# Performance work log

Hardware: AMD Instinct MI355X
Metric: run time of the kernel (lower is better)

## Reference

```python
import jax, jax.numpy as jnp
import numpy as np

B, S, D, H = 2, 2048, 1024, 16
HD = D // H  # head size = 64

def setup_inputs() -> dict:
    key = jax.random.key(0)
    ks = jax.random.split(key, 12)
    sc = 0.02
    return {
        "hidden_states": jax.random.normal(ks[0], (B, S, D), jnp.float32),
        "attention_mask": jnp.zeros((B, S), jnp.float32),  # additive mask (0 = attend)
        "position_bias": jax.random.normal(ks[1], (H, S, S), jnp.float32) * sc,
        "Wq": jax.random.normal(ks[2], (D, D), jnp.float32) * sc,
        "bq": jnp.zeros((D,), jnp.float32),
        "Wk": jax.random.normal(ks[3], (D, D), jnp.float32) * sc,
        "bk": jnp.zeros((D,), jnp.float32),
        "Wv": jax.random.normal(ks[4], (D, D), jnp.float32) * sc,
        "bv": jnp.zeros((D,), jnp.float32),
        "Wo": jax.random.normal(ks[5], (D, D), jnp.float32) * sc,
        "bo": jnp.zeros((D,), jnp.float32),
    }

def reference(hidden_states, attention_mask, position_bias, Wq, bq, Wk, bk, Wv, bv, Wo, bo):
    b, s, _ = hidden_states.shape
    def heads(x):
        # [B,S,D] -> [B,H,S,HD]
        return x.reshape(b, s, H, HD).transpose(0, 2, 1, 3)
    q = heads(hidden_states @ Wq + bq)
    k = heads(hidden_states @ Wk + bk)
    v = heads(hidden_states @ Wv + bv)
    scores = jnp.einsum("bhqd,bhkd->bhqk", q, k) / jnp.sqrt(jnp.float32(HD))
    scores = scores + position_bias[None]                 # [1,H,S,S]
    scores = scores + attention_mask[:, None, None, :]    # [B,1,1,S]
    probs = jax.nn.softmax(scores, axis=-1)
    # dropout is identity in eval mode
    ctx = jnp.einsum("bhqk,bhkd->bhqd", probs, v)
    ctx = ctx.transpose(0, 2, 1, 3).reshape(b, s, D)
    return ctx @ Wo + bo
```

## Files before the change

### kernel.cpp

```cpp
#include <hip/hip_runtime.h>
#include <hip/hip_bf16.h>

#define B_  2
#define S_  2048
#define D_  1024
#define H_  16
#define HD_ 64
#define M_  (B_ * S_)

typedef unsigned short u16;
typedef __attribute__((ext_vector_type(8))) short short8;
typedef __attribute__((ext_vector_type(4))) float f32x4;

#define MFMA16(a, b, c) __builtin_amdgcn_mfma_f32_16x16x32_bf16(a, b, c, 0, 0, 0)

__device__ __forceinline__ u16 f2bf(float f) {
    union { float f; unsigned u; } v; v.f = f;
    unsigned r = v.u + 0x7FFFu + ((v.u >> 16) & 1u);
    return (u16)(r >> 16);
}

__device__ __forceinline__ void gl_lds16(const void* g, void* lds) {
    __builtin_amdgcn_global_load_lds(
        (const __attribute__((address_space(1))) unsigned int*)g,
        (__attribute__((address_space(3))) unsigned int*)lds, 16, 0, 0);
}

__global__ __launch_bounds__(256) void cvt_bf16(const float* __restrict__ x,
                                                u16* __restrict__ y) {
    const int i = (blockIdx.x * 256 + threadIdx.x) * 4;
    const float4 v = *(const float4*)(x + i);
    ushort4 o;
    o.x = f2bf(v.x); o.y = f2bf(v.y); o.z = f2bf(v.z); o.w = f2bf(v.w);
    *(ushort4*)(y + i) = o;
}

__global__ __launch_bounds__(256) void wt_trans(
    const float* __restrict__ w0, const float* __restrict__ w1,
    const float* __restrict__ w2, const float* __restrict__ w3,
    u16* __restrict__ t0, u16* __restrict__ t1,
    u16* __restrict__ t2, u16* __restrict__ t3) {
    const float* W; u16* T;
    switch (blockIdx.z) {
        case 0: W = w0; T = t0; break;
        case 1: W = w1; T = t1; break;
        case 2: W = w2; T = t2; break;
        default: W = w3; T = t3; break;
    }
    __shared__ float t[32][33];
    const int tid = threadIdx.x;
    const int kt = blockIdx.x, nt = blockIdx.y;
    const int r = tid >> 3, c4 = (tid & 7) * 4;
    const float4 v = *(const float4*)&W[(size_t)(kt * 32 + r) * D_ + nt * 32 + c4];
    t[c4 + 0][r] = v.x; t[c4 + 1][r] = v.y; t[c4 + 2][r] = v.z; t[c4 + 3][r] = v.w;
    __syncthreads();
    ushort4 o;
    o.x = f2bf(t[r][c4 + 0]); o.y = f2bf(t[r][c4 + 1]);
    o.z = f2bf(t[r][c4 + 2]); o.w = f2bf(t[r][c4 + 3]);
    *(ushort4*)&T[(size_t)(nt * 32 + r) * D_ + kt * 32 + c4] = o;
}

__global__ __launch_bounds__(256) void v_trans(const u16* __restrict__ V,
                                               u16* __restrict__ VT) {
    __shared__ u16 t[64][72];
    const int bh = blockIdx.x, s0 = blockIdx.y * 64;
    const int tid = threadIdx.x;
    const int ss = tid >> 2, cq = tid & 3;
    const u16* src = V + ((size_t)bh * S_ + s0 + ss) * HD_ + cq * 16;
    u16 buf[16];
    *(uint4*)&buf[0] = *(const uint4*)&src[0];
    *(uint4*)&buf[8] = *(const uint4*)&src[8];
#pragma unroll
    for (int j = 0; j < 16; ++j) t[cq * 16 + j][ss] = buf[j];
    __syncthreads();
    const int dd = tid >> 2;
    u16 ob[16];
#pragma unroll
    for (int j = 0; j < 16; ++j) ob[j] = t[dd][cq * 16 + j];
    u16* dst = VT + ((size_t)bh * HD_ + dd) * S_ + s0 + cq * 16;
    *(uint4*)&dst[0] = *(uint4*)&ob[0];
    *(uint4*)&dst[8] = *(uint4*)&ob[8];
}

__global__ __launch_bounds__(256, 3) void gemm_bt_bf16(
    const u16* __restrict__ A, const u16* __restrict__ Bt,
    const float* __restrict__ bi0, const float* __restrict__ bi1, const float* __restrict__ bi2,
    void* __restrict__ o0, void* __restrict__ o1, void* __restrict__ o2,
    int mode) {
    __shared__ __align__(16) char smem[32768];

    const int tid = threadIdx.x;
    const int wave = tid >> 6, lane = tid & 63;
    const int quad = lane >> 4, l15 = lane & 15;
    const int wm = wave >> 1, wn = wave & 1;
    const int bm = blockIdx.x * 128, bn = blockIdx.y * 128;

    const int sel = bn >> 10;
    const float* bias = (sel == 0) ? bi0 : (sel == 1) ? bi1 : bi2;
    void* outp = (sel == 0) ? o0 : (sel == 1) ? o1 : o2;

    f32x4 acc[4][4];
#pragma unroll
    for (int i = 0; i < 4; ++i)
#pragma unroll
        for (int j = 0; j < 4; ++j) acc[i][j] = (f32x4)0.f;

    const int c0 = wave * 128 + lane;
#pragma unroll
    for (int i = 0; i < 2; ++i) {
        const int c = c0 + i * 64;
        const int row = c >> 2, e = c & 3;
        gl_lds16(A  + (size_t)(bm + row) * D_ + e * 8,
                 smem + (wave * 2 + i) * 1024);
        gl_lds16(Bt + (size_t)(bn + row) * D_ + e * 8,
                 smem + 16384 + (wave * 2 + i) * 1024);
    }
    __syncthreads();

    for (int it = 0; it < 32; ++it) {
        const int cur = it & 1;
        if (it < 31) {
            const int k0n = (it + 1) * 32;
            const int nb = cur ^ 1;
#pragma unroll
            for (int i = 0; i < 2; ++i) {
                const int c = c0 + i * 64;
                const int row = c >> 2, e = c & 3;
                gl_lds16(A  + (size_t)(bm + row) * D_ + k0n + e * 8,
                         smem + nb * 8192 + (wave * 2 + i) * 1024);
                gl_lds16(Bt + (size_t)(bn + row) * D_ + k0n + e * 8,
                         smem + 16384 + nb * 8192 + (wave * 2 + i) * 1024);
            }
        }

        short8 aF[4], bF[4];
#pragma unroll
        for (int mt = 0; mt < 4; ++mt)
            aF[mt] = *(const short8*)(smem + cur * 8192 +
                     ((wm * 64 + mt * 16 + l15) * 32 + quad * 8) * 2);
#pragma unroll
        for (int nt = 0; nt < 4; ++nt)
            bF[nt] = *(const short8*)(smem + 16384 + cur * 8192 +
                     ((wn * 64 + nt * 16 + l15) * 32 + quad * 8) * 2);
#pragma unroll
        for (int mt = 0; mt < 4; ++mt)
#pragma unroll
            for (int nt = 0; nt < 4; ++nt)
                acc[mt][nt] = MFMA16(aF[mt], bF[nt], acc[mt][nt]);

        __syncthreads();
    }

    float bv[4];
#pragma unroll
    for (int nt = 0; nt < 4; ++nt)
        bv[nt] = bias[(bn & 1023) + wn * 64 + nt * 16 + l15];

    if (mode == 1) {
        u16* ob = (u16*)outp;
#pragma unroll
        for (int mt = 0; mt < 4; ++mt)
#pragma unroll
            for (int nt = 0; nt < 4; ++nt)
#pragma unroll
                for (int r = 0; r < 4; ++r) {
                    const int m = bm + wm * 64 + mt * 16 + quad * 4 + r;
                    const int n = (bn & 1023) + wn * 64 + nt * 16 + l15;
                    const int bb = m >> 11, ss = m & (S_ - 1);
                    const int hh = n >> 6,  dd = n & (HD_ - 1);
                    ob[(((size_t)bb * H_ + hh) * S_ + ss) * HD_ + dd] =
                        f2bf(acc[mt][nt][r] + bv[nt]);
                }
    } else {
        float* of = (float*)outp;
#pragma unroll
        for (int mt = 0; mt < 4; ++mt)
#pragma unroll
            for (int nt = 0; nt < 4; ++nt)
#pragma unroll
                for (int r = 0; r < 4; ++r) {
                    const int m = bm + wm * 64 + mt * 16 + quad * 4 + r;
                    const int n = bn + wn * 64 + nt * 16 + l15;
                    of[(size_t)m * D_ + n] = acc[mt][nt][r] + bv[nt];
                }
    }
}

#define AQP_OFF 0
#define AK_OFF  8192
#define AV_OFF  24576

__global__ __launch_bounds__(256, 4) void attn_mfma(
    const u16* __restrict__ Qg, const u16* __restrict__ Kg, const u16* __restrict__ VTg,
    const float* __restrict__ pb, const float* __restrict__ mask,
    u16* __restrict__ Cb) {
    __shared__ __align__(16) char smem[40960];
    u16* PsU = (u16*)(smem + AQP_OFF);

    const int tid = threadIdx.x;
    const int wave = tid >> 6, lane = tid & 63;
    const int quad = lane >> 4, l15 = lane & 15;

    const int b = blockIdx.x & 1, qblk = blockIdx.x >> 1;
    const int h = blockIdx.y;
    const int q0 = qblk * 64;

    const size_t bh = (size_t)b * H_ + h;
    const u16* Qb  = Qg  + bh * (S_ * HD_);
    const u16* Kb  = Kg  + bh * (S_ * HD_);
    const u16* VTb = VTg + bh * (HD_ * S_);

#pragma unroll
    for (int i = 0; i < 2; ++i) {
        const int c = (wave * 2 + i) * 64 + lane;
        const int row = c >> 3, e = c & 7, dc = e ^ (row & 7);
        gl_lds16(Qb + (size_t)(q0 + row) * HD_ + dc * 8,
                 smem + AQP_OFF + (wave * 2 + i) * 1024);
        gl_lds16(Kb + (size_t)row * HD_ + dc * 8,
                 smem + AK_OFF + (wave * 2 + i) * 1024);
        gl_lds16(VTb + (size_t)row * S_ + dc * 8,
                 smem + AV_OFF + (wave * 2 + i) * 1024);
    }
    __syncthreads();

    short8 aQ[2];
#pragma unroll
    for (int kc = 0; kc < 2; ++kc) {
        const int q = wave * 16 + l15;
        const int dc = kc * 4 + quad;
        aQ[kc] = *(const short8*)(smem + AQP_OFF + (q * 8 + (dc ^ (q & 7))) * 16);
    }

    u16* Pw = PsU + (l15 >> 3) * 512 + (wave * 16 + quad * 4) * 8 + (l15 & 7);

    f32x4 O[4];
    float lst[4];
#pragma unroll
    for (int nt = 0; nt < 4; ++nt) O[nt] = (f32x4)0.f;
#pragma unroll
    for (int r = 0; r < 4; ++r) lst[r] = 0.f;

    for (int kt = 0; kt < S_ / 64; ++kt) {
        const int k0 = kt * 64;
        const int cur = kt & 1;

        if (kt < S_ / 64 - 1) {
            const int nb = cur ^ 1;
            const int k0n = k0 + 64;
#pragma unroll
            for (int i = 0; i < 2; ++i) {
                const int c = (wave * 2 + i) * 64 + lane;
                const int row = c >> 3, e = c & 7, dc = e ^ (row & 7);
                gl_lds16(Kb + (size_t)(k0n + row) * HD_ + dc * 8,
                         smem + AK_OFF + nb * 8192 + (wave * 2 + i) * 1024);
                gl_lds16(VTb + (size_t)row * S_ + k0n + dc * 8,
                         smem + AV_OFF + nb * 8192 + (wave * 2 + i) * 1024);
            }
        }

        float mk[4], pbv[4][4];
#pragma unroll
        for (int nt = 0; nt < 4; ++nt) mk[nt] = mask[b * S_ + k0 + nt * 16 + l15];
#pragma unroll
        for (int r = 0; r < 4; ++r) {
            const int qg = q0 + wave * 16 + quad * 4 + r;
            const float* rowp = pb + ((size_t)h * S_ + qg) * S_ + k0;
#pragma unroll
            for (int nt = 0; nt < 4; ++nt) pbv[r][nt] = rowp[nt * 16 + l15];
        }

        f32x4 sc[4];
#pragma unroll
        for (int nt = 0; nt < 4; ++nt) sc[nt] = (f32x4)0.f;
#pragma unroll
        for (int nt = 0; nt < 4; ++nt)
#pragma unroll
            for (int kc = 0; kc < 2; ++kc) {
                const int kk = nt * 16 + l15;
                const int dc = kc * 4 + quad;
                const short8 bK = *(const short8*)(smem + AK_OFF + cur * 8192 +
                                   (kk * 8 + (dc ^ (kk & 7))) * 16);
                sc[nt] = MFMA16(aQ[kc], bK, sc[nt]);
            }

#pragma unroll
        for (int r = 0; r < 4; ++r) {
            const float s0 = fmaf(sc[0][r], 0.125f, pbv[r][0] + mk[0]);
            const float s1 = fmaf(sc[1][r], 0.125f, pbv[r][1] + mk[1]);
            const float s2 = fmaf(sc[2][r], 0.125f, pbv[r][2] + mk[2]);
            const float s3 = fmaf(sc[3][r], 0.125f, pbv[r][3] + mk[3]);
            const float p0 = __expf(s0), p1 = __expf(s1);
            const float p2 = __expf(s2), p3 = __expf(s3);
            lst[r] += (p0 + p1) + (p2 + p3);
            Pw[0 * 1024 + r * 8] = f2bf(p0);
            Pw[1 * 1024 + r * 8] = f2bf(p1);
            Pw[2 * 1024 + r * 8] = f2bf(p2);
            Pw[3 * 1024 + r * 8] = f2bf(p3);
        }

        short8 aP[2];
#pragma unroll
        for (int kc = 0; kc < 2; ++kc)
            aP[kc] = *(const short8*)(PsU + (kc * 4 + quad) * 512 + (wave * 16 + l15) * 8);
#pragma unroll
        for (int nt = 0; nt < 4; ++nt)
#pragma unroll
            for (int kc = 0; kc < 2; ++kc) {
                const int d = nt * 16 + l15;
                const int dc = kc * 4 + quad;
                const short8 bV = *(const short8*)(smem + AV_OFF + cur * 8192 +
                                   (d * 8 + (dc ^ (d & 7))) * 16);
                O[nt] = MFMA16(aP[kc], bV, O[nt]);
            }

        __syncthreads();
    }

#pragma unroll
    for (int r = 0; r < 4; ++r) {
#pragma unroll
        for (int off = 1; off < 16; off <<= 1)
            lst[r] += __shfl_xor(lst[r], off, 64);
        const float inv = 1.f / lst[r];
        const int s = q0 + wave * 16 + quad * 4 + r;
        u16* dst = Cb + ((size_t)b * S_ + s) * D_ + h * HD_;
#pragma unroll
        for (int nt = 0; nt < 4; ++nt)
            dst[nt * 16 + l15] = f2bf(O[nt][r] * inv);
    }
}

extern "C" void kernel_launch(void* const* d_in, const int* in_sizes, int n_in,
                              void* d_out, int out_size, void* d_ws, size_t ws_size,
                              hipStream_t stream) {
    const float* X    = (const float*)d_in[0];
    const float* mask = (const float*)d_in[1];
    const float* pb   = (const float*)d_in[2];
    const float* Wq   = (const float*)d_in[3];
    const float* bq   = (const float*)d_in[4];
    const float* Wk   = (const float*)d_in[5];
    const float* bk   = (const float*)d_in[6];
    const float* Wv   = (const float*)d_in[7];
    const float* bv   = (const float*)d_in[8];
    const float* Wo   = (const float*)d_in[9];
    const float* bo   = (const float*)d_in[10];
    float* out = (float*)d_out;

    u16* Xb    = (u16*)d_ws;
    u16* WtQKV = Xb    + (size_t)M_ * D_;
    u16* Wto   = WtQKV + (size_t)3 * D_ * D_;
    u16* Qw    = Wto   + (size_t)D_ * D_;
    u16* Kw    = Qw    + (size_t)M_ * D_;
    u16* Vw    = Kw    + (size_t)M_ * D_;
    u16* Cb    = Vw    + (size_t)M_ * D_;
    u16* VTw   = Cb    + (size_t)M_ * D_;

    cvt_bf16<<<(M_ * D_) / (256 * 4), 256, 0, stream>>>(X, Xb);
    wt_trans<<<dim3(32, 32, 4), 256, 0, stream>>>(
        Wq, Wk, Wv, Wo, WtQKV, WtQKV + (size_t)D_ * D_, WtQKV + (size_t)2 * D_ * D_, Wto);

    gemm_bt_bf16<<<dim3(M_ / 128, 3 * D_ / 128), 256, 0, stream>>>(
        Xb, WtQKV, bq, bk, bv, Qw, Kw, Vw, 1);

    v_trans<<<dim3(B_ * H_, S_ / 64), 256, 0, stream>>>(Vw, VTw);

    attn_mfma<<<dim3((S_ / 64) * B_, H_), 256, 0, stream>>>(Qw, Kw, VTw, pb, mask, Cb);

    gemm_bt_bf16<<<dim3(M_ / 128, D_ / 128), 256, 0, stream>>>(
        Cb, Wto, bo, bo, bo, out, out, out, 0);
}
```

Baseline: 510.1 us.

## Process both batch elements per attention block to share position-bias loads

The attention kernel now has each block handle the same query tile and head for both batch entries, so each position_bias tile is loaded once and used for two batches instead of being fetched twice from separate blocks. The bias and mask for the next key tile are prefetched into registers, with nontemporal loads, while the current tile is computed. LDS use grows to 72KB, launch bounds drop to 2 blocks per SM, and the grid is halved, which lowers occupancy and parallelism in exchange for halving position_bias traffic.

```diff
diff --git a/kernel.cpp b/kernel.cpp
--- a/kernel.cpp
+++ b/kernel.cpp
@@ -186,63 +186,85 @@
     }
 }
 
-#define AQP_OFF 0
-#define AK_OFF  8192
-#define AV_OFF  24576
-
-__global__ __launch_bounds__(256, 4) void attn_mfma(
+#define PS_OFF   0
+#define AK2_OFF  8192
+#define AV2_OFF  40960
+#define Q1_STAGE 32768
+
+__global__ __launch_bounds__(256, 2) void attn_mfma(
     const u16* __restrict__ Qg, const u16* __restrict__ Kg, const u16* __restrict__ VTg,
     const float* __restrict__ pb, const float* __restrict__ mask,
     u16* __restrict__ Cb) {
-    __shared__ __align__(16) char smem[40960];
-    u16* PsU = (u16*)(smem + AQP_OFF);
+    __shared__ __align__(16) char smem[73728];
+    u16* PsU = (u16*)(smem + PS_OFF);
 
     const int tid = threadIdx.x;
     const int wave = tid >> 6, lane = tid & 63;
     const int quad = lane >> 4, l15 = lane & 15;
 
-    const int b = blockIdx.x & 1, qblk = blockIdx.x >> 1;
+    const int qblk = blockIdx.x;
     const int h = blockIdx.y;
     const int q0 = qblk * 64;
 
-    const size_t bh = (size_t)b * H_ + h;
-    const u16* Qb  = Qg  + bh * (S_ * HD_);
-    const u16* Kb  = Kg  + bh * (S_ * HD_);
-    const u16* VTb = VTg + bh * (HD_ * S_);
+    const u16* Qb0 = Qg  + (size_t)h        * (S_ * HD_);
+    const u16* Qb1 = Qg  + (size_t)(H_ + h) * (S_ * HD_);
+    const u16* Kb0 = Kg  + (size_t)h        * (S_ * HD_);
+    const u16* Kb1 = Kg  + (size_t)(H_ + h) * (S_ * HD_);
+    const u16* VT0 = VTg + (size_t)h        * (HD_ * S_);
+    const u16* VT1 = VTg + (size_t)(H_ + h) * (HD_ * S_);
 
 #pragma unroll
     for (int i = 0; i < 2; ++i) {
         const int c = (wave * 2 + i) * 64 + lane;
         const int row = c >> 3, e = c & 7, dc = e ^ (row & 7);
-        gl_lds16(Qb + (size_t)(q0 + row) * HD_ + dc * 8,
-                 smem + AQP_OFF + (wave * 2 + i) * 1024);
-        gl_lds16(Kb + (size_t)row * HD_ + dc * 8,
-                 smem + AK_OFF + (wave * 2 + i) * 1024);
-        gl_lds16(VTb + (size_t)row * S_ + dc * 8,
-                 smem + AV_OFF + (wave * 2 + i) * 1024);
+        const int off = (wave * 2 + i) * 1024;
+        gl_lds16(Qb0 + (size_t)(q0 + row) * HD_ + dc * 8, smem + PS_OFF + off);
+        gl_lds16(Qb1 + (size_t)(q0 + row) * HD_ + dc * 8, smem + Q1_STAGE + off);
+        gl_lds16(Kb0 + (size_t)row * HD_ + dc * 8, smem + AK2_OFF + 0 * 8192 + off);
+        gl_lds16(Kb1 + (size_t)row * HD_ + dc * 8, smem + AK2_OFF + 1 * 8192 + off);
+        gl_lds16(VT0 + (size_t)row * S_ + dc * 8,  smem + AV2_OFF + 0 * 8192 + off);
+        gl_lds16(VT1 + (size_t)row * S_ + dc * 8,  smem + AV2_OFF + 1 * 8192 + off);
     }
     __syncthreads();
 
-    short8 aQ[2];
+    short8 aQ[2][2];
 #pragma unroll
     for (int kc = 0; kc < 2; ++kc) {
         const int q = wave * 16 + l15;
         const int dc = kc * 4 + quad;
-        aQ[kc] = *(const short8*)(smem + AQP_OFF + (q * 8 + (dc ^ (q & 7))) * 16);
+        const int boff = (q * 8 + (dc ^ (q & 7))) * 16;
+        aQ[0][kc] = *(const short8*)(smem + PS_OFF + boff);
+        aQ[1][kc] = *(const short8*)(smem + Q1_STAGE + boff);
     }
 
     u16* Pw = PsU + (l15 >> 3) * 512 + (wave * 16 + quad * 4) * 8 + (l15 & 7);
 
-    f32x4 O[4];
-    float lst[4];
-#pragma unroll
-    for (int nt = 0; nt < 4; ++nt) O[nt] = (f32x4)0.f;
-#pragma unroll
-    for (int r = 0; r < 4; ++r) lst[r] = 0.f;
+    f32x4 O[2][4];
+    float lst[2][4];
+#pragma unroll
+    for (int bb = 0; bb < 2; ++bb)
+#pragma unroll
+        for (int nt = 0; nt < 4; ++nt) { O[bb][nt] = (f32x4)0.f; lst[bb][nt] = 0.f; }
+
+    float pbc[4][4], mkc[2][4];
+#pragma unroll
+    for (int nt = 0; nt < 4; ++nt) {
+        mkc[0][nt] = mask[nt * 16 + l15];
+        mkc[1][nt] = mask[S_ + nt * 16 + l15];
+    }
+#pragma unroll
+    for (int r = 0; r < 4; ++r) {
+        const int qg = q0 + wave * 16 + quad * 4 + r;
+        const float* rowp = pb + ((size_t)h * S_ + qg) * S_;
+#pragma unroll
+        for (int nt = 0; nt < 4; ++nt)
+            pbc[r][nt] = __builtin_nontemporal_load(rowp + nt * 16 + l15);
+    }
 
     for (int kt = 0; kt < S_ / 64; ++kt) {
         const int k0 = kt * 64;
         const int cur = kt & 1;
+        float pbn[4][4], mkn[2][4];
 
         if (kt < S_ / 64 - 1) {
             const int nb = cur ^ 1;
@@ -251,83 +273,110 @@
             for (int i = 0; i < 2; ++i) {
                 const int c = (wave * 2 + i) * 64 + lane;
                 const int row = c >> 3, e = c & 7, dc = e ^ (row & 7);
-                gl_lds16(Kb + (size_t)(k0n + row) * HD_ + dc * 8,
-                         smem + AK_OFF + nb * 8192 + (wave * 2 + i) * 1024);
-                gl_lds16(VTb + (size_t)row * S_ + k0n + dc * 8,
-                         smem + AV_OFF + nb * 8192 + (wave * 2 + i) * 1024);
+                const int off = (wave * 2 + i) * 1024;
+                gl_lds16(Kb0 + (size_t)(k0n + row) * HD_ + dc * 8,
+                         smem + AK2_OFF + (nb * 2 + 0) * 8192 + off);
+                gl_lds16(Kb1 + (size_t)(k0n + row) * HD_ + dc * 8,
+                         smem + AK2_OFF + (nb * 2 + 1) * 8192 + off);
+                gl_lds16(VT0 + (size_t)row * S_ + k0n + dc * 8,
+                         smem + AV2_OFF + (nb * 2 + 0) * 8192 + off);
+                gl_lds16(VT1 + (size_t)row * S_ + k0n + dc * 8,
+                         smem + AV2_OFF + (nb * 2 + 1) * 8192 + off);
+            }
+#pragma unroll
+            for (int nt = 0; nt < 4; ++nt) {
+                mkn[0][nt] = mask[k0n + nt * 16 + l15];
+                mkn[1][nt] = mask[S_ + k0n + nt * 16 + l15];
+            }
+#pragma unroll
+            for (int r = 0; r < 4; ++r) {
+                const int qg = q0 + wave * 16 + quad * 4 + r;
+                const float* rowp = pb + ((size_t)h * S_ + qg) * S_ + k0n;
+#pragma unroll
+                for (int nt = 0; nt < 4; ++nt)
+                    pbn[r][nt] = __builtin_nontemporal_load(rowp + nt * 16 + l15);
             }
         }
 
-        float mk[4], pbv[4][4];
-#pragma unroll
-        for (int nt = 0; nt < 4; ++nt) mk[nt] = mask[b * S_ + k0 + nt * 16 + l15];
+#pragma unroll
+        for (int bb = 0; bb < 2; ++bb) {
+            const int koff = AK2_OFF + (cur * 2 + bb) * 8192;
+            const int voff = AV2_OFF + (cur * 2 + bb) * 8192;
+
+            f32x4 sc[4];
+#pragma unroll
+            for (int nt = 0; nt < 4; ++nt) sc[nt] = (f32x4)0.f;
+#pragma unroll
+            for (int nt = 0; nt < 4; ++nt)
+#pragma unroll
+                for (int kc = 0; kc < 2; ++kc) {
+                    const int kk = nt * 16 + l15;
+                    const int dc = kc * 4 + quad;
+                    const short8 bK = *(const short8*)(smem + koff +
+                                       (kk * 8 + (dc ^ (kk & 7))) * 16);
+                    sc[nt] = MFMA16(aQ[bb][kc], bK, sc[nt]);
+                }
+
+#pragma unroll
+            for (int r = 0; r < 4; ++r) {
+                const float s0 = fmaf(sc[0][r], 0.125f, pbc[r][0] + mkc[bb][0]);
+                const float s1 = fmaf(sc[1][r], 0.125f, pbc[r][1] + mkc[bb][1]);
+                const float s2 = fmaf(sc[2][r], 0.125f, pbc[r][2] + mkc[bb][2]);
+                const float s3 = fmaf(sc[3][r], 0.125f, pbc[r][3] + mkc[bb][3]);
+                const float p0 = __expf(s0), p1 = __expf(s1);
+                const float p2 = __expf(s2), p3 = __expf(s3);
+                lst[bb][r] += (p0 + p1) + (p2 + p3);
+                Pw[0 * 1024 + r * 8] = f2bf(p0);
+                Pw[1 * 1024 + r * 8] = f2bf(p1);
+                Pw[2 * 1024 + r * 8] = f2bf(p2);
+                Pw[3 * 1024 + r * 8] = f2bf(p3);
+            }
+
+            short8 aP[2];
+#pragma unroll
+            for (int kc = 0; kc < 2; ++kc)
+                aP[kc] = *(const short8*)(PsU + (kc * 4 + quad) * 512 +
+                                          (wave * 16 + l15) * 8);
+#pragma unroll
+            for (int nt = 0; nt < 4; ++nt)
+#pragma unroll
+                for (int kc = 0; kc < 2; ++kc) {
+                    const int d = nt * 16 + l15;
+                    const int dc = kc * 4 + quad;
+                    const short8 bV = *(const short8*)(smem + voff +
+                                       (d * 8 + (dc ^ (d & 7))) * 16);
+                    O[bb][nt] = MFMA16(aP[kc], bV, O[bb][nt]);
+                }
+        }
+
+        if (kt < S_ / 64 - 1) {
+#pragma unroll
+            for (int r = 0; r < 4; ++r)
+#pragma unroll
+                for (int nt = 0; nt < 4; ++nt) pbc[r][nt] = pbn[r][nt];
+#pragma unroll
+            for (int nt = 0; nt < 4; ++nt) {
+                mkc[0][nt] = mkn[0][nt]; mkc[1][nt] = mkn[1][nt];
+            }
+        }
+        __syncthreads();
+    }
+
+#pragma unroll
+    for (int bb = 0; bb < 2; ++bb)
 #pragma unroll
         for (int r = 0; r < 4; ++r) {
-            const int qg = q0 + wave * 16 + quad * 4 + r;
-            const float* rowp = pb + ((size_t)h * S_ + qg) * S_ + k0;
-#pragma unroll
-            for (int nt = 0; nt < 4; ++nt) pbv[r][nt] = rowp[nt * 16 + l15];
+            float l = lst[bb][r];
+#pragma unroll
+            for (int off = 1; off < 16; off <<= 1)
+                l += __shfl_xor(l, off, 64);
+            const float inv = 1.f / l;
+            const int s = q0 + wave * 16 + quad * 4 + r;
+            u16* dst = Cb + ((size_t)bb * S_ + s) * D_ + h * HD_;
+#pragma unroll
+            for (int nt = 0; nt < 4; ++nt)
+                dst[nt * 16 + l15] = f2bf(O[bb][nt][r] * inv);
         }
-
-        f32x4 sc[4];
-#pragma unroll
-        for (int nt = 0; nt < 4; ++nt) sc[nt] = (f32x4)0.f;
-#pragma unroll
-        for (int nt = 0; nt < 4; ++nt)
-#pragma unroll
-            for (int kc = 0; kc < 2; ++kc) {
-                const int kk = nt * 16 + l15;
-                const int dc = kc * 4 + quad;
-                const short8 bK = *(const short8*)(smem + AK_OFF + cur * 8192 +
-                                   (kk * 8 + (dc ^ (kk & 7))) * 16);
-                sc[nt] = MFMA16(aQ[kc], bK, sc[nt]);
-            }
-
-#pragma unroll
-        for (int r = 0; r < 4; ++r) {
-            const float s0 = fmaf(sc[0][r], 0.125f, pbv[r][0] + mk[0]);
-            const float s1 = fmaf(sc[1][r], 0.125f, pbv[r][1] + mk[1]);
-            const float s2 = fmaf(sc[2][r], 0.125f, pbv[r][2] + mk[2]);
-            const float s3 = fmaf(sc[3][r], 0.125f, pbv[r][3] + mk[3]);
-            const float p0 = __expf(s0), p1 = __expf(s1);
-            const float p2 = __expf(s2), p3 = __expf(s3);
-            lst[r] += (p0 + p1) + (p2 + p3);
-            Pw[0 * 1024 + r * 8] = f2bf(p0);
-            Pw[1 * 1024 + r * 8] = f2bf(p1);
-            Pw[2 * 1024 + r * 8] = f2bf(p2);
-            Pw[3 * 1024 + r * 8] = f2bf(p3);
-        }
-
-        short8 aP[2];
-#pragma unroll
-        for (int kc = 0; kc < 2; ++kc)
-            aP[kc] = *(const short8*)(PsU + (kc * 4 + quad) * 512 + (wave * 16 + l15) * 8);
-#pragma unroll
-        for (int nt = 0; nt < 4; ++nt)
-#pragma unroll
-            for (int kc = 0; kc < 2; ++kc) {
-                const int d = nt * 16 + l15;
-                const int dc = kc * 4 + quad;
-                const short8 bV = *(const short8*)(smem + AV_OFF + cur * 8192 +
-                                   (d * 8 + (dc ^ (d & 7))) * 16);
-                O[nt] = MFMA16(aP[kc], bV, O[nt]);
-            }
-
-        __syncthreads();
-    }
-
-#pragma unroll
-    for (int r = 0; r < 4; ++r) {
-#pragma unroll
-        for (int off = 1; off < 16; off <<= 1)
-            lst[r] += __shfl_xor(lst[r], off, 64);
-        const float inv = 1.f / lst[r];
-        const int s = q0 + wave * 16 + quad * 4 + r;
-        u16* dst = Cb + ((size_t)b * S_ + s) * D_ + h * HD_;
-#pragma unroll
-        for (int nt = 0; nt < 4; ++nt)
-            dst[nt * 16 + l15] = f2bf(O[nt][r] * inv);
-    }
 }
 
 extern "C" void kernel_launch(void* const* d_in, const int* in_sizes, int n_in,
@@ -364,7 +413,7 @@
 
     v_trans<<<dim3(B_ * H_, S_ / 64), 256, 0, stream>>>(Vw, VTw);
 
-    attn_mfma<<<dim3((S_ / 64) * B_, H_), 256, 0, stream>>>(Qw, Kw, VTw, pb, mask, Cb);
+    attn_mfma<<<dim3(S_ / 64, H_), 256, 0, stream>>>(Qw, Kw, VTw, pb, mask, Cb);
 
     gemm_bt_bf16<<<dim3(M_ / 128, D_ / 128), 256, 0, stream>>>(
         Cb, Wto, bo, bo, bo, out, out, out, 0);
```

After: 477.4 us. 6.4% less time.
